# Kernel optimization log

Hardware: AMD Instinct MI355X
Metric: run time of the kernel (lower is better)

The kernel has to match this reference:

```python
import jax, jax.numpy as jnp
import numpy as np

N_NODES = 50000
N_EDGES = 1600000
F_IN = 384
NR_SIGMOID = 1  # hidden_sizes[-1]


def setup_inputs() -> dict:
    key = jax.random.key(0)
    ks = jax.random.split(key, 8)
    x = jax.random.normal(ks[0], (N_NODES, F_IN), jnp.float32)
    edge_index = jax.random.randint(ks[1], (2, N_EDGES), 0, N_NODES, jnp.int32)
    def lin(k, fin, fout):
        return jax.random.normal(k, (fin, fout), jnp.float32) / np.sqrt(fin).astype(np.float32)
    W1 = lin(ks[2], F_IN, 64)
    W2 = lin(ks[3], 64, 32)
    W3 = lin(ks[4], 32, 1 + F_IN)  # reconstruction=True: last width = 1 + input_size
    return {
        "x": x, "edge_index": edge_index,
        "W1": W1, "b1": jnp.zeros((64,), jnp.float32),
        "W2": W2, "b2": jnp.zeros((32,), jnp.float32),
        "W3": W3, "b3": jnp.zeros((1 + F_IN,), jnp.float32),
    }


def reference(x, edge_index, W1, b1, W2, b2, W3, b3):
    N = x.shape[0]
    self_loop = jnp.arange(N, dtype=edge_index.dtype)
    src = jnp.concatenate([edge_index[0], self_loop])  # [E+N]
    dst = jnp.concatenate([edge_index[1], self_loop])
    # symmetric GCN normalization (with self-loops), as in PyG GCNConv
    deg = jax.ops.segment_sum(jnp.ones(dst.shape[0], x.dtype), dst, num_segments=N)
    dinv = jnp.where(deg > 0, jax.lax.rsqrt(deg), 0.0)
    norm = (dinv[src] * dinv[dst])[:, None]  # [E+N, 1]

    def gcn_conv(h, W, b):
        m = h @ W                         # transform first (fewer message bytes)
        agg = jax.ops.segment_sum(m[src] * norm, dst, num_segments=N)
        return agg + b

    h = jax.nn.relu(gcn_conv(x, W1, b1))
    h = jax.nn.relu(gcn_conv(h, W2, b2))
    h = gcn_conv(h, W3, b3)
    # sigmoid on the first nr_sigmoid_layers columns only
    return jnp.concatenate([jax.nn.sigmoid(h[:, :NR_SIGMOID]), h[:, NR_SIGMOID:]], axis=1)
```

## Files before the change

kernel.cpp:

```cpp
#include <hip/hip_runtime.h>

#define F_IN  384
#define EPB   4096
#define NBINS 256
#define BCAP  10240
#define SDS   208

typedef __attribute__((ext_vector_type(8))) short short8v;
typedef __attribute__((ext_vector_type(4))) float f32x4;

__device__ __forceinline__ unsigned short f2bf(float f) {
    unsigned u = __float_as_uint(f);
    return (unsigned short)((u + 0x7FFFu + ((u >> 16) & 1u)) >> 16);
}
__device__ __forceinline__ float bflo(unsigned u) { return __uint_as_float(u << 16); }
__device__ __forceinline__ float bfhi(unsigned u) { return __uint_as_float(u & 0xFFFF0000u); }


__launch_bounds__(256)
__global__ void k_p1(const int* __restrict__ ei, int E, int NBK,
                     unsigned* __restrict__ packed, unsigned short* __restrict__ segdesc) {
    __shared__ unsigned sin[EPB];
    __shared__ unsigned sout[EPB];
    __shared__ int hist[257], cur[256], excl[257];
    const int t = threadIdx.x;
    const int e0 = blockIdx.x * EPB;
    const int cnt = min(EPB, E - e0);

    if (t < 256) { hist[t] = 0; cur[t] = 0; }
    if (t == 0) hist[256] = 0;
    __syncthreads();

    for (int i = t; i < cnt; i += 256) {
        int s = ei[e0 + i];
        int d = ei[E + e0 + i];
        sin[i] = ((unsigned)d << 16) | (unsigned)s;
        atomicAdd(&hist[d >> 8], 1);
    }
    __syncthreads();

    if (t < 64) {
        int carry = 0;
        for (int c = 0; c * 64 < NBK; ++c) {
            int idx = c * 64 + t;
            int v = (idx < NBK) ? hist[idx] : 0;
            int x = v;
#pragma unroll
            for (int d = 1; d < 64; d <<= 1) { int y = __shfl_up(x, d, 64); if (t >= d) x += y; }
            if (idx < NBK) excl[idx] = carry + x - v;
            carry += __shfl(x, 63, 64);
        }
        if (t == 0) excl[NBK] = carry;
    }
    __syncthreads();

    for (int i = t; i < cnt; i += 256) {
        unsigned v = sin[i];
        int b = v >> 24;
        int pos = excl[b] + atomicAdd(&cur[b], 1);
        sout[pos] = v;
    }
    __syncthreads();

    for (int i = t; i < cnt; i += 256) packed[(size_t)e0 + i] = sout[i];
    for (int i = t; i <= NBK; i += 256) segdesc[(size_t)blockIdx.x * SDS + i] = (unsigned short)excl[i];
}


__launch_bounds__(256)
__global__ void k_p2(const unsigned* __restrict__ packed, const unsigned short* __restrict__ segdesc,
                     int NB1, unsigned short* __restrict__ eidx,
                     int* __restrict__ rpB, int* __restrict__ rpE,
                     float* __restrict__ dinv, int N) {
    __shared__ unsigned ev[BCAP];
    __shared__ unsigned short se[BCAP];
    __shared__ int lenS[512], offS[513], srcS[512];
    __shared__ int hist[NBINS], cur[NBINS], excl[NBINS + 1];
    const int t = threadIdx.x;
    const int b = blockIdx.x;

    if (t < NBINS) { hist[t] = 0; cur[t] = 0; }
    for (int blk = t; blk < NB1; blk += 256) {
        int s0 = segdesc[(size_t)blk * SDS + b];
        int s1 = segdesc[(size_t)blk * SDS + b + 1];
        lenS[blk] = s1 - s0;
        srcS[blk] = s0;
    }
    __syncthreads();

    if (t < 64) {
        int carry = 0;
        for (int c = 0; c * 64 < NB1; ++c) {
            int idx = c * 64 + t;
            int v = (idx < NB1) ? lenS[idx] : 0;
            int x = v;
#pragma unroll
            for (int d = 1; d < 64; d <<= 1) { int y = __shfl_up(x, d, 64); if (t >= d) x += y; }
            if (idx < NB1) offS[idx] = carry + x - v;
            carry += __shfl(x, 63, 64);
        }
        if (t == 0) offS[NB1 < 512 ? NB1 : 512] = carry;
    }
    __syncthreads();
    const int total = min(offS[NB1 < 512 ? NB1 : 512], BCAP);

    for (int blk = t; blk < NB1; blk += 256) {
        int l = lenS[blk], o = offS[blk];
        if (o + l > BCAP) l = max(0, BCAP - o);
        const unsigned* sp = packed + (size_t)blk * EPB + srcS[blk];
        for (int j = 0; j < l; ++j) ev[o + j] = sp[j];
    }
    __syncthreads();

    for (int i = t; i < total; i += 256) atomicAdd(&hist[(ev[i] >> 16) & 0xFF], 1);
    __syncthreads();

    if (t < 64) {
        int carry = 0;
#pragma unroll
        for (int c = 0; c < 4; ++c) {
            int idx = c * 64 + t;
            int v = hist[idx];
            int x = v;
#pragma unroll
            for (int d = 1; d < 64; d <<= 1) { int y = __shfl_up(x, d, 64); if (t >= d) x += y; }
            excl[idx] = carry + x - v;
            carry += __shfl(x, 63, 64);
        }
        if (t == 0) excl[NBINS] = carry;
    }
    __syncthreads();

    if (t < NBINS) {
        int d = b * NBINS + t;
        if (d < N) {
            int c = hist[t];
            int base = b * BCAP + excl[t];
            rpB[d] = base;
            rpE[d] = base + c;
            dinv[d] = rsqrtf((float)(c + 1));
        }
    }
    for (int i = t; i < total; i += 256) {
        unsigned v = ev[i];
        int l = (v >> 16) & 0xFF;
        int p = excl[l] + atomicAdd(&cur[l], 1);
        se[p] = (unsigned short)(v & 0xFFFF);
    }
    __syncthreads();
    for (int i = t; i < total; i += 256) eidx[(size_t)b * BCAP + i] = se[i];
}


__global__ void k_wt(const float* __restrict__ W1, const float* __restrict__ W3,
                     unsigned short* __restrict__ w1t, unsigned short* __restrict__ w3t) {
    int idx = blockIdx.x * 256 + threadIdx.x;
    if (idx < 384 * 64) {
        int k = idx >> 6, col = idx & 63;
        w1t[(size_t)col * 384 + k] = f2bf(W1[idx]);
    }
    int j = idx - 384 * 64;
    if (j >= 0 && j < 384 * 32) {
        int col = j >> 5, k = j & 31;
        w3t[(size_t)col * 32 + k] = f2bf(W3[(size_t)k * 385 + col]);
    }
}


__launch_bounds__(256)
__global__ void k_gemm1(const float* __restrict__ x, const unsigned short* __restrict__ w1t,
                        const float* __restrict__ dinv,
                        unsigned short* __restrict__ m1p, int N) {
    const int t    = threadIdx.x;
    const int lane = t & 63;
    const int wv   = t >> 6;
    const int lr   = lane & 15;
    const int kg   = lane >> 4;
    const int row0 = blockIdx.x * 32;
    const int col  = (wv << 4) + lr;

    short8v bf[12];
    const unsigned short* wcol = w1t + (size_t)col * 384 + (kg << 3);
#pragma unroll
    for (int c = 0; c < 12; c++)
        bf[c] = *reinterpret_cast<const short8v*>(&wcol[c * 32]);

    const int r0 = row0 + lr;
    const int r1 = row0 + 16 + lr;
    const bool has0 = (r0 < N), has1 = (r1 < N);
    const float* p0 = x + (size_t)r0 * 384 + (kg << 3);
    const float* p1 = x + (size_t)r1 * 384 + (kg << 3);

    f32x4 acc0 = (f32x4){0.f, 0.f, 0.f, 0.f};
    f32x4 acc1 = (f32x4){0.f, 0.f, 0.f, 0.f};

#pragma unroll
    for (int c = 0; c < 12; c++) {
        short8v a0 = (short8v){0, 0, 0, 0, 0, 0, 0, 0};
        short8v a1 = (short8v){0, 0, 0, 0, 0, 0, 0, 0};
        if (has0) {
            float4 f0 = *reinterpret_cast<const float4*>(p0 + c * 32);
            float4 f1 = *reinterpret_cast<const float4*>(p0 + c * 32 + 4);
            a0[0] = (short)f2bf(f0.x); a0[1] = (short)f2bf(f0.y);
            a0[2] = (short)f2bf(f0.z); a0[3] = (short)f2bf(f0.w);
            a0[4] = (short)f2bf(f1.x); a0[5] = (short)f2bf(f1.y);
            a0[6] = (short)f2bf(f1.z); a0[7] = (short)f2bf(f1.w);
        }
        if (has1) {
            float4 f0 = *reinterpret_cast<const float4*>(p1 + c * 32);
            float4 f1 = *reinterpret_cast<const float4*>(p1 + c * 32 + 4);
            a1[0] = (short)f2bf(f0.x); a1[1] = (short)f2bf(f0.y);
            a1[2] = (short)f2bf(f0.z); a1[3] = (short)f2bf(f0.w);
            a1[4] = (short)f2bf(f1.x); a1[5] = (short)f2bf(f1.y);
            a1[6] = (short)f2bf(f1.z); a1[7] = (short)f2bf(f1.w);
        }
        acc0 = __builtin_amdgcn_mfma_f32_16x16x32_bf16(a0, bf[c], acc0, 0, 0, 0);
        acc1 = __builtin_amdgcn_mfma_f32_16x16x32_bf16(a1, bf[c], acc1, 0, 0, 0);
    }

    const size_t hbase = (size_t)(col >> 5) * ((size_t)N * 32) + (col & 31);
#pragma unroll
    for (int i = 0; i < 4; i++) {
        int rowA = row0 + (kg << 2) + i;
        if (rowA < N) m1p[hbase + (size_t)rowA * 32] = f2bf(acc0[i] * dinv[rowA]);
        int rowB = row0 + 16 + (kg << 2) + i;
        if (rowB < N) m1p[hbase + (size_t)rowB * 32] = f2bf(acc1[i] * dinv[rowB]);
    }
}


__launch_bounds__(256)
__global__ void k_g64half(const int* __restrict__ rpB, const int* __restrict__ rpE,
                          const unsigned short* __restrict__ eidx,
                          const unsigned* __restrict__ msg,
                          const float* __restrict__ b1h,
                          const float* __restrict__ dinv,
                          unsigned* __restrict__ m1h,
                          int houtoff, int N) {
    int w = blockIdx.x * 16 + (threadIdx.x >> 4);
    if (w >= N) return;
    int f = threadIdx.x & 15;
    int i = rpB[w], e = rpE[w];
    unsigned u = msg[(size_t)w * 16 + f];
    float l0 = bflo(u), h0 = bfhi(u);
    float l1 = 0.f, h1 = 0.f, l2 = 0.f, h2 = 0.f, l3 = 0.f, h3 = 0.f;
    float l4 = 0.f, h4 = 0.f, l5 = 0.f, h5 = 0.f, l6 = 0.f, h6 = 0.f, l7 = 0.f, h7 = 0.f;
    for (; i + 8 <= e; i += 8) {
        unsigned u0 = msg[(size_t)eidx[i]     * 16 + f];
        unsigned u1 = msg[(size_t)eidx[i + 1] * 16 + f];
        unsigned u2 = msg[(size_t)eidx[i + 2] * 16 + f];
        unsigned u3 = msg[(size_t)eidx[i + 3] * 16 + f];
        unsigned u4 = msg[(size_t)eidx[i + 4] * 16 + f];
        unsigned u5 = msg[(size_t)eidx[i + 5] * 16 + f];
        unsigned u6 = msg[(size_t)eidx[i + 6] * 16 + f];
        unsigned u7 = msg[(size_t)eidx[i + 7] * 16 + f];
        l0 += bflo(u0); h0 += bfhi(u0);  l1 += bflo(u1); h1 += bfhi(u1);
        l2 += bflo(u2); h2 += bfhi(u2);  l3 += bflo(u3); h3 += bfhi(u3);
        l4 += bflo(u4); h4 += bfhi(u4);  l5 += bflo(u5); h5 += bfhi(u5);
        l6 += bflo(u6); h6 += bfhi(u6);  l7 += bflo(u7); h7 += bfhi(u7);
    }
    for (; i + 4 <= e; i += 4) {
        unsigned u0 = msg[(size_t)eidx[i]     * 16 + f];
        unsigned u1 = msg[(size_t)eidx[i + 1] * 16 + f];
        unsigned u2 = msg[(size_t)eidx[i + 2] * 16 + f];
        unsigned u3 = msg[(size_t)eidx[i + 3] * 16 + f];
        l0 += bflo(u0); h0 += bfhi(u0);  l1 += bflo(u1); h1 += bfhi(u1);
        l2 += bflo(u2); h2 += bfhi(u2);  l3 += bflo(u3); h3 += bfhi(u3);
    }
    for (; i < e; i++) {
        unsigned u0 = msg[(size_t)eidx[i] * 16 + f];
        l0 += bflo(u0); h0 += bfhi(u0);
    }
    float suml = ((l0 + l1) + (l2 + l3)) + ((l4 + l5) + (l6 + l7));
    float sumh = ((h0 + h1) + (h2 + h3)) + ((h4 + h5) + (h6 + h7));
    float s = dinv[w];
    float hl = fmaxf(suml * s + b1h[(f << 1)], 0.f);
    float hh = fmaxf(sumh * s + b1h[(f << 1) + 1], 0.f);
    m1h[(size_t)w * 32 + houtoff + f] = (unsigned)f2bf(hl) | ((unsigned)f2bf(hh) << 16);
}


__launch_bounds__(256)
__global__ void k_gather32h(const int* __restrict__ rpB, const int* __restrict__ rpE,
                            const unsigned short* __restrict__ eidx,
                            const unsigned* __restrict__ msg,
                            void* __restrict__ outp, int N,
                            const float* __restrict__ bias, const float* __restrict__ dinv,
                            const float* __restrict__ W3, const float* __restrict__ b3,
                            float* __restrict__ out) {
    int w = blockIdx.x * 16 + (threadIdx.x >> 4);
    if (w >= N) return;
    int f = threadIdx.x & 15;
    int i = rpB[w], e = rpE[w];
    unsigned u = msg[(size_t)w * 16 + f];
    float l0 = bflo(u), h0 = bfhi(u);
    float l1 = 0.f, h1 = 0.f, l2 = 0.f, h2 = 0.f, l3 = 0.f, h3 = 0.f;
    float l4 = 0.f, h4 = 0.f, l5 = 0.f, h5 = 0.f, l6 = 0.f, h6 = 0.f, l7 = 0.f, h7 = 0.f;
    for (; i + 8 <= e; i += 8) {
        unsigned u0 = msg[(size_t)eidx[i]     * 16 + f];
        unsigned u1 = msg[(size_t)eidx[i + 1] * 16 + f];
        unsigned u2 = msg[(size_t)eidx[i + 2] * 16 + f];
        unsigned u3 = msg[(size_t)eidx[i + 3] * 16 + f];
        unsigned u4 = msg[(size_t)eidx[i + 4] * 16 + f];
        unsigned u5 = msg[(size_t)eidx[i + 5] * 16 + f];
        unsigned u6 = msg[(size_t)eidx[i + 6] * 16 + f];
        unsigned u7 = msg[(size_t)eidx[i + 7] * 16 + f];
        l0 += bflo(u0); h0 += bfhi(u0);  l1 += bflo(u1); h1 += bfhi(u1);
        l2 += bflo(u2); h2 += bfhi(u2);  l3 += bflo(u3); h3 += bfhi(u3);
        l4 += bflo(u4); h4 += bfhi(u4);  l5 += bflo(u5); h5 += bfhi(u5);
        l6 += bflo(u6); h6 += bfhi(u6);  l7 += bflo(u7); h7 += bfhi(u7);
    }
    for (; i + 4 <= e; i += 4) {
        unsigned u0 = msg[(size_t)eidx[i]     * 16 + f];
        unsigned u1 = msg[(size_t)eidx[i + 1] * 16 + f];
        unsigned u2 = msg[(size_t)eidx[i + 2] * 16 + f];
        unsigned u3 = msg[(size_t)eidx[i + 3] * 16 + f];
        l0 += bflo(u0); h0 += bfhi(u0);  l1 += bflo(u1); h1 += bfhi(u1);
        l2 += bflo(u2); h2 += bfhi(u2);  l3 += bflo(u3); h3 += bfhi(u3);
    }
    for (; i < e; i++) {
        unsigned u0 = msg[(size_t)eidx[i] * 16 + f];
        l0 += bflo(u0); h0 += bfhi(u0);
    }
    float rl = ((l0 + l1) + (l2 + l3)) + ((l4 + l5) + (l6 + l7));
    float rh = ((h0 + h1) + (h2 + h3)) + ((h4 + h5) + (h6 + h7));
    float s = dinv[w];
    if (bias) {
        rl = fmaxf(rl * s + bias[(f << 1)], 0.f) * s;
        rh = fmaxf(rh * s + bias[(f << 1) + 1], 0.f) * s;
        ((unsigned*)outp)[(size_t)w * 16 + f] = (unsigned)f2bf(rl) | ((unsigned)f2bf(rh) << 16);
    } else {
        float gl = rl * s, gh = rh * s;
        ((unsigned*)outp)[(size_t)w * 16 + f] = (unsigned)f2bf(gl) | ((unsigned)f2bf(gh) << 16);
        float p = gl * W3[(size_t)(2 * f) * 385 + 384] + gh * W3[(size_t)(2 * f + 1) * 385 + 384];
#pragma unroll
        for (int m = 8; m >= 1; m >>= 1) p += __shfl_xor(p, m, 64);
        if (f == 0) out[(size_t)w * 385 + 384] = p + b3[384];
    }
}


__launch_bounds__(256)
__global__ void k_layer2(const unsigned* __restrict__ m1h, const float* __restrict__ W2,
                         const float* __restrict__ dinv,
                         unsigned short* __restrict__ m2p, int N) {
    const int t    = threadIdx.x;
    const int lane = t & 63;
    const int wv   = t >> 6;
    const int lr   = lane & 15;
    const int kg   = lane >> 4;
    const int row0 = blockIdx.x * 64 + (wv << 4);

    short8v b00, b01, b10, b11;
#pragma unroll
    for (int j = 0; j < 8; j++) {
        int k = (kg << 3) + j;
        b00[j] = (short)f2bf(W2[(size_t)k * 32 + lr]);
        b01[j] = (short)f2bf(W2[(size_t)k * 32 + 16 + lr]);
        b10[j] = (short)f2bf(W2[(size_t)(32 + k) * 32 + lr]);
        b11[j] = (short)f2bf(W2[(size_t)(32 + k) * 32 + 16 + lr]);
    }

    int arow = row0 + lr;
    short8v a0 = (short8v){0, 0, 0, 0, 0, 0, 0, 0};
    short8v a1 = (short8v){0, 0, 0, 0, 0, 0, 0, 0};
    if (arow < N) {
        a0 = *reinterpret_cast<const short8v*>(&m1h[(size_t)arow * 32 + (kg << 2)]);
        a1 = *reinterpret_cast<const short8v*>(&m1h[(size_t)arow * 32 + 16 + (kg << 2)]);
    }

    f32x4 accA = (f32x4){0.f, 0.f, 0.f, 0.f};
    f32x4 accB = (f32x4){0.f, 0.f, 0.f, 0.f};
    accA = __builtin_amdgcn_mfma_f32_16x16x32_bf16(a0, b00, accA, 0, 0, 0);
    accA = __builtin_amdgcn_mfma_f32_16x16x32_bf16(a1, b10, accA, 0, 0, 0);
    accB = __builtin_amdgcn_mfma_f32_16x16x32_bf16(a0, b01, accB, 0, 0, 0);
    accB = __builtin_amdgcn_mfma_f32_16x16x32_bf16(a1, b11, accB, 0, 0, 0);

#pragma unroll
    for (int i = 0; i < 4; i++) {
        int row = row0 + (kg << 2) + i;
        if (row < N) {
            float s = dinv[row];
            m2p[(size_t)row * 32 + lr]      = f2bf(accA[i] * s);
            m2p[(size_t)row * 32 + 16 + lr] = f2bf(accB[i] * s);
        }
    }
}


__launch_bounds__(256)
__global__ void k_out(const unsigned* __restrict__ gbf, const unsigned short* __restrict__ w3t,
                      const float* __restrict__ b3, float* __restrict__ out, int N) {
    const int t    = threadIdx.x;
    const int lane = t & 63;
    const int wv   = t >> 6;
    const int lr   = lane & 15;
    const int kg   = lane >> 4;
    const int row0 = blockIdx.x * 64;
    const int col  = blockIdx.y * 64 + (wv << 4) + lr;

    short8v bfrag = *reinterpret_cast<const short8v*>(&w3t[(size_t)col * 32 + (kg << 3)]);
    const float bias = b3[col];

#pragma unroll
    for (int rb = 0; rb < 4; rb++) {
        int arow = row0 + (rb << 4) + lr;
        short8v afrag = (short8v){0, 0, 0, 0, 0, 0, 0, 0};
        if (arow < N)
            afrag = *reinterpret_cast<const short8v*>(&gbf[(size_t)arow * 16 + (kg << 2)]);
        f32x4 acc = (f32x4){0.f, 0.f, 0.f, 0.f};
        acc = __builtin_amdgcn_mfma_f32_16x16x32_bf16(afrag, bfrag, acc, 0, 0, 0);
#pragma unroll
        for (int i = 0; i < 4; i++) {
            int row = row0 + (rb << 4) + (kg << 2) + i;
            if (row < N) {
                float v = acc[i] + bias;
                if (col == 0) v = 1.0f / (1.0f + expf(-v));
                out[(size_t)row * 385 + col] = v;
            }
        }
    }
}

extern "C" void kernel_launch(void* const* d_in, const int* in_sizes, int n_in,
                              void* d_out, int out_size, void* d_ws, size_t ws_size,
                              hipStream_t stream) {
    const float* x  = (const float*)d_in[0];
    const int*   ei = (const int*)d_in[1];
    const float* W1 = (const float*)d_in[2];
    const float* b1 = (const float*)d_in[3];
    const float* W2 = (const float*)d_in[4];
    const float* b2 = (const float*)d_in[5];
    const float* W3 = (const float*)d_in[6];
    const float* b3 = (const float*)d_in[7];
    float* out = (float*)d_out;

    const int N = in_sizes[0] / F_IN;
    const int E = in_sizes[1] / 2;
    const int NB1 = (E + EPB - 1) / EPB;
    const int NBK = (N + NBINS - 1) / NBINS;

    float* ws   = (float*)d_ws;
    float* dinv = ws;
    float* bufA = ws + N;
    float* bufB = bufA + (size_t)64 * N;
    int*   rpB  = (int*)(bufB + (size_t)64 * N);
    int*   rpE  = rpB + N;
    unsigned short* eidx    = (unsigned short*)(rpE + N);
    unsigned short* segdesc = eidx + (size_t)NBK * BCAP;
    unsigned short* w1t     = segdesc + (size_t)NB1 * SDS;
    unsigned short* w3t     = w1t + (size_t)64 * 384;

    unsigned* packed = (unsigned*)bufA;
    unsigned short* m1p = (unsigned short*)bufA;
    unsigned* m1h = (unsigned*)bufB;
    unsigned short* m2p = (unsigned short*)bufA;
    unsigned short* h2p = (unsigned short*)bufB;
    unsigned* gbf = (unsigned*)(bufA + (size_t)32 * N);

    k_p1<<<NB1, 256, 0, stream>>>(ei, E, NBK, packed, segdesc);
    k_p2<<<NBK, 256, 0, stream>>>(packed, segdesc, NB1, eidx, rpB, rpE, dinv, N);
    k_wt<<<(384 * 64 + 384 * 32 + 255) / 256, 256, 0, stream>>>(W1, W3, w1t, w3t);

    k_gemm1  <<<(N + 31) / 32, 256, 0, stream>>>(x, w1t, dinv, m1p, N);
    k_g64half<<<(N + 15) / 16, 256, 0, stream>>>(rpB, rpE, eidx,
                                                 (const unsigned*)m1p,                       b1,      dinv, m1h,  0, N);
    k_g64half<<<(N + 15) / 16, 256, 0, stream>>>(rpB, rpE, eidx,
                                                 (const unsigned*)(m1p + (size_t)N * 32),    b1 + 32, dinv, m1h, 16, N);

    k_layer2  <<<(N + 63) / 64, 256, 0, stream>>>(m1h, W2, dinv, m2p, N);
    k_gather32h<<<(N + 15) / 16, 256, 0, stream>>>(rpB, rpE, eidx, (const unsigned*)m2p,
                                                   (void*)h2p, N, b2, dinv, nullptr, nullptr, nullptr);

    k_gather32h<<<(N + 15) / 16, 256, 0, stream>>>(rpB, rpE, eidx, (const unsigned*)h2p,
                                                   (void*)gbf, N, nullptr, dinv, W3, b3, out);

    dim3 gout((N + 63) / 64, 6);
    k_out<<<gout, 256, 0, stream>>>(gbf, w3t, b3, out, N);
}
```

Measured before the change: 179.8 us.

## Stage x tile through shared memory in gemm1 with register prefetch

Before this change, each of the four waves loaded and converted the full 32x384 x tile on its own, so every x element was read and bf16-converted four times. Now the block loads each 32x128 chunk cooperatively once, converts it to bf16 into padded LDS, and the waves read MFMA operands from LDS. The next chunk is prefetched into registers while the current one is processed. This cuts redundant global loads and conversions at the cost of LDS traffic and two barriers per chunk.

```diff
diff --git a/kernel.cpp b/kernel.cpp
--- a/kernel.cpp
+++ b/kernel.cpp
@@ -171,6 +171,7 @@
 __global__ void k_gemm1(const float* __restrict__ x, const unsigned short* __restrict__ w1t,
                         const float* __restrict__ dinv,
                         unsigned short* __restrict__ m1p, int N) {
+    __shared__ __align__(16) unsigned short xb[32][136];
     const int t    = threadIdx.x;
     const int lane = t & 63;
     const int wv   = t >> 6;
@@ -185,37 +186,61 @@
     for (int c = 0; c < 12; c++)
         bf[c] = *reinterpret_cast<const short8v*>(&wcol[c * 32]);
 
-    const int r0 = row0 + lr;
-    const int r1 = row0 + 16 + lr;
-    const bool has0 = (r0 < N), has1 = (r1 < N);
-    const float* p0 = x + (size_t)r0 * 384 + (kg << 3);
-    const float* p1 = x + (size_t)r1 * 384 + (kg << 3);
+    int sr[2], sk[2];
+    const float* sp[2];
+    bool sv[2];
+#pragma unroll
+    for (int i = 0; i < 2; i++) {
+        int g = t + i * 256;
+        sr[i] = g >> 4;
+        sk[i] = (g & 15) << 3;
+        int row = row0 + sr[i];
+        sv[i] = (row < N);
+        sp[i] = x + (size_t)row * F_IN + sk[i];
+    }
+
+    float4 preA0, preA1, preB0, preB1;
+    preA0 = sv[0] ? *reinterpret_cast<const float4*>(sp[0])     : make_float4(0, 0, 0, 0);
+    preA1 = sv[0] ? *reinterpret_cast<const float4*>(sp[0] + 4) : make_float4(0, 0, 0, 0);
+    preB0 = sv[1] ? *reinterpret_cast<const float4*>(sp[1])     : make_float4(0, 0, 0, 0);
+    preB1 = sv[1] ? *reinterpret_cast<const float4*>(sp[1] + 4) : make_float4(0, 0, 0, 0);
 
     f32x4 acc0 = (f32x4){0.f, 0.f, 0.f, 0.f};
     f32x4 acc1 = (f32x4){0.f, 0.f, 0.f, 0.f};
 
-#pragma unroll
-    for (int c = 0; c < 12; c++) {
-        short8v a0 = (short8v){0, 0, 0, 0, 0, 0, 0, 0};
-        short8v a1 = (short8v){0, 0, 0, 0, 0, 0, 0, 0};
-        if (has0) {
-            float4 f0 = *reinterpret_cast<const float4*>(p0 + c * 32);
-            float4 f1 = *reinterpret_cast<const float4*>(p0 + c * 32 + 4);
-            a0[0] = (short)f2bf(f0.x); a0[1] = (short)f2bf(f0.y);
-            a0[2] = (short)f2bf(f0.z); a0[3] = (short)f2bf(f0.w);
-            a0[4] = (short)f2bf(f1.x); a0[5] = (short)f2bf(f1.y);
-            a0[6] = (short)f2bf(f1.z); a0[7] = (short)f2bf(f1.w);
-        }
-        if (has1) {
-            float4 f0 = *reinterpret_cast<const float4*>(p1 + c * 32);
-            float4 f1 = *reinterpret_cast<const float4*>(p1 + c * 32 + 4);
-            a1[0] = (short)f2bf(f0.x); a1[1] = (short)f2bf(f0.y);
-            a1[2] = (short)f2bf(f0.z); a1[3] = (short)f2bf(f0.w);
-            a1[4] = (short)f2bf(f1.x); a1[5] = (short)f2bf(f1.y);
-            a1[6] = (short)f2bf(f1.z); a1[7] = (short)f2bf(f1.w);
-        }
-        acc0 = __builtin_amdgcn_mfma_f32_16x16x32_bf16(a0, bf[c], acc0, 0, 0, 0);
-        acc1 = __builtin_amdgcn_mfma_f32_16x16x32_bf16(a1, bf[c], acc1, 0, 0, 0);
+    for (int k0 = 0; k0 < F_IN; k0 += 128) {
+        __syncthreads();
+        {
+            short8v p;
+            p[0] = (short)f2bf(preA0.x); p[1] = (short)f2bf(preA0.y);
+            p[2] = (short)f2bf(preA0.z); p[3] = (short)f2bf(preA0.w);
+            p[4] = (short)f2bf(preA1.x); p[5] = (short)f2bf(preA1.y);
+            p[6] = (short)f2bf(preA1.z); p[7] = (short)f2bf(preA1.w);
+            *reinterpret_cast<short8v*>(&xb[sr[0]][sk[0]]) = p;
+            p[0] = (short)f2bf(preB0.x); p[1] = (short)f2bf(preB0.y);
+            p[2] = (short)f2bf(preB0.z); p[3] = (short)f2bf(preB0.w);
+            p[4] = (short)f2bf(preB1.x); p[5] = (short)f2bf(preB1.y);
+            p[6] = (short)f2bf(preB1.z); p[7] = (short)f2bf(preB1.w);
+            *reinterpret_cast<short8v*>(&xb[sr[1]][sk[1]]) = p;
+        }
+        if (k0 + 128 < F_IN) {
+            const float* q0 = sp[0] + k0 + 128;
+            const float* q1 = sp[1] + k0 + 128;
+            preA0 = sv[0] ? *reinterpret_cast<const float4*>(q0)     : make_float4(0, 0, 0, 0);
+            preA1 = sv[0] ? *reinterpret_cast<const float4*>(q0 + 4) : make_float4(0, 0, 0, 0);
+            preB0 = sv[1] ? *reinterpret_cast<const float4*>(q1)     : make_float4(0, 0, 0, 0);
+            preB1 = sv[1] ? *reinterpret_cast<const float4*>(q1 + 4) : make_float4(0, 0, 0, 0);
+        }
+        __syncthreads();
+
+#pragma unroll
+        for (int kk = 0; kk < 4; kk++) {
+            const int c = (k0 >> 5) + kk;
+            short8v a0 = *reinterpret_cast<const short8v*>(&xb[lr][(kk << 5) + (kg << 3)]);
+            short8v a1 = *reinterpret_cast<const short8v*>(&xb[16 + lr][(kk << 5) + (kg << 3)]);
+            acc0 = __builtin_amdgcn_mfma_f32_16x16x32_bf16(a0, bf[c], acc0, 0, 0, 0);
+            acc1 = __builtin_amdgcn_mfma_f32_16x16x32_bf16(a1, bf[c], acc1, 0, 0, 0);
+        }
     }
 
     const size_t hbase = (size_t)(col >> 5) * ((size_t)N * 32) + (col & 31);
```

Result: faster. 151.0 us (-16.1%).
